# Optimization experiments

Measured on AMD Instinct MI355X. Metric: run time of the kernel, lower is better.

Reference implementation:

```python
import jax, jax.numpy as jnp
import numpy as np

N = 4096          # n_nodes
M = 8192          # m_nodes (= 2*N, required by block structure)
D = 128           # in_dim == hidden_dim (conv1 is reapplied to its own output)
H = 128
NUM_ITERS = 3


def setup_inputs() -> dict:
    key = jax.random.key(0)
    ks = jax.random.split(key, 6)
    X = jax.random.normal(ks[0], (N, D), dtype=jnp.float32)
    R = jax.random.uniform(ks[1], (N, N), dtype=jnp.float32)
    A = 0.5 * (R + R.T)  # symmetric, strictly positive connectivity matrix
    # upsample MLP: Linear(n_nodes -> m_nodes - n_nodes), torch weight layout [out, in]
    W_up = jax.random.normal(ks[2], (M - N, N), dtype=jnp.float32) * 0.02
    b_up = jnp.zeros((M - N,), dtype=jnp.float32)
    # GCNConv linear weights stored [in, out]
    W1 = jax.random.normal(ks[3], (D, H), dtype=jnp.float32) * 0.05
    b1 = jnp.zeros((H,), dtype=jnp.float32)
    W2 = jax.random.normal(ks[4], (H, H), dtype=jnp.float32) * 0.05
    b2 = jnp.zeros((H,), dtype=jnp.float32)
    return dict(X=X, A=A, W_up=W_up, b_up=b_up, W1=W1, b1=b1, W2=W2, b2=b2)


def _gcn(Adj, X, W, b):
    # PyG GCNConv on a fully dense, strictly-positive weighted graph:
    # every diagonal entry is nonzero, so add_remaining_self_loops is a no-op and
    # out = D^{-1/2} A D^{-1/2} (X W) + b  exactly.
    deg = Adj.sum(axis=0)                         # [m] column degree
    dinv = jnp.where(deg > 0, jax.lax.rsqrt(deg), 0.0)
    An = Adj * dinv[:, None] * dinv[None, :]      # symmetric normalization
    return An @ (X @ W) + b


def reference(X, A, W_up, b_up, W1, b1, W2, b2):
    # new_nodes = upsample_mlp(X.T).T  -> [M-N, D]
    new_nodes = (X.T @ W_up.T + b_up).T
    Xu = jnp.concatenate([X, new_nodes], axis=0)  # [M, D]
    # block adjacency: [[A, A.T], [A, sigmoid(new @ new.T)]]
    Adj = jnp.block([[A, A.T],
                     [A, jax.nn.sigmoid(new_nodes @ new_nodes.T)]])  # [M, M]
    A_out = Adj
    for _ in range(NUM_ITERS):
        Xu = jax.nn.relu(_gcn(Adj, Xu, W1, b1))
        Adj = jax.nn.sigmoid(Xu @ Xu.T)           # mid-loop adjacency rebuild
        Xu = jax.nn.relu(_gcn(Adj, Xu, W2, b2))
        A_out = jax.nn.sigmoid(Xu @ Xu.T)
        # NOTE: edge_index for the next conv1 is NOT rebuilt from A_out in the
        # original (only after conv1), so Adj carries the mid-loop matrix.
    return A_out
```

## Files before the change

### kernel.cpp

```cpp
#include <hip/hip_runtime.h>
#include <hip/hip_bf16.h>


#define N_NODES 4096
#define M_NODES 8192
#define DIM 128
#define SPLITS 8

typedef __attribute__((ext_vector_type(4))) float f32x4;
typedef __attribute__((ext_vector_type(8))) short bf16x8;

__device__ __forceinline__ unsigned short f2bf(float f) {
  union { float f; unsigned u; } v; v.f = f;
  unsigned r = v.u + 0x7fffu + ((v.u >> 16) & 1u);
  return (unsigned short)(r >> 16);
}

__device__ __forceinline__ void gld16(unsigned short* lds, const unsigned short* g) {
  __builtin_amdgcn_global_load_lds(
      (const __attribute__((address_space(1))) unsigned int*)g,
      (__attribute__((address_space(3))) unsigned int*)lds, 16, 0, 0);
}

__device__ __forceinline__ float sigmoidf_(float x) { return 1.0f / (1.0f + __expf(-x)); }


__global__ void cast_x_kernel(const float* __restrict__ X, unsigned short* __restrict__ Xu,
                              unsigned short* __restrict__ XT) {
  int idx = blockIdx.x * 256 + threadIdx.x;
  int i = idx >> 7, c = idx & 127;
  unsigned short b = f2bf(X[idx]);
  Xu[idx] = b;
  XT[(size_t)c * N_NODES + i] = b;
}

__global__ void cast_wup_kernel(const float4* __restrict__ W, ushort4* __restrict__ Wb) {
  int idx = blockIdx.x * 256 + threadIdx.x;
  float4 v = W[idx];
  ushort4 o;
  o.x = f2bf(v.x); o.y = f2bf(v.y); o.z = f2bf(v.z); o.w = f2bf(v.w);
  Wb[idx] = o;
}

__global__ void cast_wt_kernel(const float* __restrict__ W, unsigned short* __restrict__ WT) {
  int idx = blockIdx.x * 256 + threadIdx.x;
  int k = idx >> 7, c = idx & 127;
  WT[c * DIM + k] = f2bf(W[idx]);
}

__global__ void cast_a_kernel(const float* __restrict__ A, unsigned short* __restrict__ Adj,
                              float* __restrict__ colsumA) {
  int c = blockIdx.x * 256 + threadIdx.x;
  int r0 = blockIdx.y * 128;
  float s = 0.f;
  for (int r = 0; r < 128; ++r) {
    int row = r0 + r;
    float a = A[(size_t)row * N_NODES + c];
    unsigned short b = f2bf(a);
    Adj[(size_t)row * M_NODES + c] = b;
    Adj[(size_t)(row + N_NODES) * M_NODES + c] = b;
    Adj[(size_t)row * M_NODES + N_NODES + c] = b;
    s += a;
  }
  atomicAdd(&colsumA[c], s);
}

__global__ void init_deg_kernel(const float* __restrict__ colsumA, float* __restrict__ deg) {
  int i = blockIdx.x * 256 + threadIdx.x;
  deg[i] = (i < N_NODES) ? 2.0f * colsumA[i] : colsumA[i - N_NODES];
}

__global__ void dinv_kernel(const float* __restrict__ deg, float* __restrict__ dinv) {
  int i = blockIdx.x * 256 + threadIdx.x;
  float d = deg[i];
  dinv[i] = d > 0.f ? rsqrtf(d) : 0.f;
}


__global__ __launch_bounds__(256)
void gemm_split_kernel(const unsigned short* __restrict__ A, long lda,
                       const unsigned short* __restrict__ BT, long ldb,
                       float* __restrict__ accOut, int M, int kChunk) {
  __shared__ __align__(16) unsigned short lA[128 * 32];
  __shared__ __align__(16) unsigned short lB[128 * 32];
  const int t = threadIdx.x;
  const int w = t >> 6, lane = t & 63;
  const int q = lane >> 4, l15 = lane & 15;
  const int m0 = blockIdx.x * 128;
  const long k0b = (long)blockIdx.y * kChunk;
  const int arow = t >> 2, achk = t & 3;

  f32x4 acc[2][8];
#pragma unroll
  for (int a = 0; a < 2; ++a)
#pragma unroll
    for (int b = 0; b < 8; ++b) acc[a][b] = (f32x4)0.f;

  for (int ks = 0; ks < kChunk; ks += 32) {
    const long k0 = k0b + ks;
    __syncthreads();
    gld16(&lA[(size_t)t * 8], &A[(size_t)(m0 + arow) * lda + k0 + achk * 8]);
    gld16(&lA[2048 + (size_t)t * 8], &A[(size_t)(m0 + 64 + arow) * lda + k0 + achk * 8]);
    gld16(&lB[(size_t)t * 8], &BT[(size_t)arow * ldb + k0 + achk * 8]);
    gld16(&lB[2048 + (size_t)t * 8], &BT[(size_t)(64 + arow) * ldb + k0 + achk * 8]);
    __syncthreads();
    bf16x8 a0 = *(const bf16x8*)&lA[(w * 32 + l15) * 32 + q * 8];
    bf16x8 a1 = *(const bf16x8*)&lA[(w * 32 + 16 + l15) * 32 + q * 8];
#pragma unroll
    for (int nt = 0; nt < 8; ++nt) {
      bf16x8 b = *(const bf16x8*)&lB[(nt * 16 + l15) * 32 + q * 8];
      acc[0][nt] = __builtin_amdgcn_mfma_f32_16x16x32_bf16(a0, b, acc[0][nt], 0, 0, 0);
      acc[1][nt] = __builtin_amdgcn_mfma_f32_16x16x32_bf16(a1, b, acc[1][nt], 0, 0, 0);
    }
  }
  float* slice = accOut + (size_t)blockIdx.y * M * DIM;
#pragma unroll
  for (int mt = 0; mt < 2; ++mt)
#pragma unroll
    for (int nt = 0; nt < 8; ++nt)
#pragma unroll
      for (int i = 0; i < 4; ++i) {
        int row = m0 + w * 32 + mt * 16 + q * 4 + i;
        slice[(size_t)row * DIM + nt * 16 + l15] = acc[mt][nt][i];
      }
}

__global__ void reduce_acc_kernel(const float* __restrict__ acc, int M,
                                  unsigned short* __restrict__ dst,
                                  const float* __restrict__ bias_row,
                                  const float* __restrict__ bias_col,
                                  const float* __restrict__ dinv, int mode) {
  int idx = blockIdx.x * 256 + threadIdx.x;
  float s = 0.f;
#pragma unroll
  for (int sp = 0; sp < SPLITS; ++sp) s += acc[(size_t)sp * M * DIM + idx];
  int row = idx >> 7, c = idx & 127;
  float v;
  if (mode == 0) v = s + bias_row[row];
  else { v = dinv[row] * s + bias_col[c]; v = fmaxf(v, 0.f); }
  dst[idx] = f2bf(v);
}


template <int MODE>
__global__ __launch_bounds__(256)
void rebuild_kernel(const unsigned short* __restrict__ XA,
                    const unsigned short* __restrict__ XB,
                    void* __restrict__ out, long ldo, float* __restrict__ deg) {
  __shared__ __align__(16) unsigned short smem[32768];
  __shared__ float lcol[128];
  unsigned short* lA = smem;
  unsigned short* lB = smem + 16384;
  const int t = threadIdx.x, w = t >> 6, lane = t & 63;
  const int q = lane >> 4, l15 = lane & 15;
  const int i0 = blockIdx.x * 128, j0 = blockIdx.y * 128;
  const int srow = t >> 2, schk = t & 3;
#pragma unroll
  for (int kk = 0; kk < 4; ++kk)
#pragma unroll
    for (int h = 0; h < 2; ++h) {
      gld16(&lA[kk * 4096 + h * 2048 + t * 8],
            &XA[(size_t)(i0 + h * 64 + srow) * DIM + kk * 32 + schk * 8]);
      gld16(&lB[kk * 4096 + h * 2048 + t * 8],
            &XB[(size_t)(j0 + h * 64 + srow) * DIM + kk * 32 + schk * 8]);
    }
  if (MODE == 0 && t < 128) lcol[t] = 0.f;
  __syncthreads();

  f32x4 acc[2][8];
#pragma unroll
  for (int a = 0; a < 2; ++a)
#pragma unroll
    for (int b = 0; b < 8; ++b) acc[a][b] = (f32x4)0.f;

#pragma unroll
  for (int kk = 0; kk < 4; ++kk) {
    bf16x8 a0 = *(const bf16x8*)&lA[kk * 4096 + (w * 32 + l15) * 32 + q * 8];
    bf16x8 a1 = *(const bf16x8*)&lA[kk * 4096 + (w * 32 + 16 + l15) * 32 + q * 8];
#pragma unroll
    for (int nt = 0; nt < 8; ++nt) {
      bf16x8 b = *(const bf16x8*)&lB[kk * 4096 + (nt * 16 + l15) * 32 + q * 8];
      acc[0][nt] = __builtin_amdgcn_mfma_f32_16x16x32_bf16(a0, b, acc[0][nt], 0, 0, 0);
      acc[1][nt] = __builtin_amdgcn_mfma_f32_16x16x32_bf16(a1, b, acc[1][nt], 0, 0, 0);
    }
  }
  __syncthreads();

  if (MODE == 0) {
    unsigned short* lC = smem;
#pragma unroll
    for (int mt = 0; mt < 2; ++mt)
#pragma unroll
      for (int nt = 0; nt < 8; ++nt) {
        float cs = 0.f;
#pragma unroll
        for (int i = 0; i < 4; ++i) {
          float sv = sigmoidf_(acc[mt][nt][i]);
          cs += sv;
          lC[(w * 32 + mt * 16 + q * 4 + i) * 136 + nt * 16 + l15] = f2bf(sv);
        }
        cs += __shfl_xor(cs, 16);
        cs += __shfl_xor(cs, 32);
        if (lane < 16) atomicAdd(&lcol[nt * 16 + lane], cs);
      }
    __syncthreads();
    unsigned short* og = (unsigned short*)out;
#pragma unroll
    for (int cc = 0; cc < 8; ++cc) {
      int ch = t + cc * 256;
      int row = ch >> 4, c16 = ch & 15;
      *(bf16x8*)&og[(size_t)(i0 + row) * ldo + j0 + c16 * 8] =
          *(const bf16x8*)&lC[row * 136 + c16 * 8];
    }
    if (t < 128) atomicAdd(&deg[j0 + t], lcol[t]);
  } else {
    float* og = (float*)out;
#pragma unroll
    for (int mt = 0; mt < 2; ++mt)
#pragma unroll
      for (int nt = 0; nt < 8; ++nt)
#pragma unroll
        for (int i = 0; i < 4; ++i)
          og[(size_t)(i0 + w * 32 + mt * 16 + q * 4 + i) * ldo + j0 + nt * 16 + l15] =
              sigmoidf_(acc[mt][nt][i]);
  }
}


__global__ __launch_bounds__(256)
void yz_kernel(const unsigned short* __restrict__ Xu, const unsigned short* __restrict__ WT,
               const float* __restrict__ dinv, unsigned short* __restrict__ ZT, int ldz) {
  __shared__ __align__(16) unsigned short smem[32768];
  unsigned short* lA = smem;
  unsigned short* lB = smem + 16384;
  const int t = threadIdx.x, w = t >> 6, lane = t & 63;
  const int q = lane >> 4, l15 = lane & 15;
  const int r0 = blockIdx.x * 128;
  const int srow = t >> 2, schk = t & 3;
#pragma unroll
  for (int kk = 0; kk < 4; ++kk)
#pragma unroll
    for (int h = 0; h < 2; ++h) {
      gld16(&lA[kk * 4096 + h * 2048 + t * 8],
            &Xu[(size_t)(r0 + h * 64 + srow) * DIM + kk * 32 + schk * 8]);
      gld16(&lB[kk * 4096 + h * 2048 + t * 8],
            &WT[(size_t)(h * 64 + srow) * DIM + kk * 32 + schk * 8]);
    }
  __syncthreads();

  f32x4 acc[2][8];
#pragma unroll
  for (int a = 0; a < 2; ++a)
#pragma unroll
    for (int b = 0; b < 8; ++b) acc[a][b] = (f32x4)0.f;

#pragma unroll
  for (int kk = 0; kk < 4; ++kk) {
    bf16x8 a0 = *(const bf16x8*)&lA[kk * 4096 + (w * 32 + l15) * 32 + q * 8];
    bf16x8 a1 = *(const bf16x8*)&lA[kk * 4096 + (w * 32 + 16 + l15) * 32 + q * 8];
#pragma unroll
    for (int nt = 0; nt < 8; ++nt) {
      bf16x8 b = *(const bf16x8*)&lB[kk * 4096 + (nt * 16 + l15) * 32 + q * 8];
      acc[0][nt] = __builtin_amdgcn_mfma_f32_16x16x32_bf16(a0, b, acc[0][nt], 0, 0, 0);
      acc[1][nt] = __builtin_amdgcn_mfma_f32_16x16x32_bf16(a1, b, acc[1][nt], 0, 0, 0);
    }
  }
  __syncthreads();
  unsigned short* lT = smem;
#pragma unroll
  for (int mt = 0; mt < 2; ++mt)
#pragma unroll
    for (int nt = 0; nt < 8; ++nt)
#pragma unroll
      for (int i = 0; i < 4; ++i) {
        int r = w * 32 + mt * 16 + q * 4 + i;
        lT[(nt * 16 + l15) * 136 + r] = f2bf(dinv[r0 + r] * acc[mt][nt][i]);
      }
  __syncthreads();
#pragma unroll
  for (int cc = 0; cc < 8; ++cc) {
    int ch = t + cc * 256;
    int c = ch >> 4, c16 = ch & 15;
    *(bf16x8*)&ZT[(size_t)c * ldz + r0 + c16 * 8] = *(const bf16x8*)&lT[c * 136 + c16 * 8];
  }
}


extern "C" void kernel_launch(void* const* d_in, const int* in_sizes, int n_in,
                              void* d_out, int out_size, void* d_ws, size_t ws_size,
                              hipStream_t stream) {
  (void)in_sizes; (void)n_in; (void)out_size;
  const float* X   = (const float*)d_in[0];
  const float* A   = (const float*)d_in[1];
  const float* Wup = (const float*)d_in[2];
  const float* bup = (const float*)d_in[3];
  const float* W1  = (const float*)d_in[4];
  const float* b1  = (const float*)d_in[5];
  const float* W2  = (const float*)d_in[6];
  const float* b2  = (const float*)d_in[7];

  const size_t ADJ_BYTES = (size_t)M_NODES * M_NODES * 2;
  char* ws = (char*)d_ws;
  size_t off = 0;
  auto alloc = [&](size_t bytes) {
    char* p = ws + off;
    off += (bytes + 255) & ~(size_t)255;
    return p;
  };
  float*          accb    = (float*)alloc((size_t)SPLITS * M_NODES * DIM * 4);
  unsigned short* Xu      = (unsigned short*)alloc((size_t)M_NODES * DIM * 2);
  unsigned short* ZT      = (unsigned short*)alloc((size_t)DIM * M_NODES * 2);
  unsigned short* XT      = (unsigned short*)alloc((size_t)DIM * N_NODES * 2);
  unsigned short* W1T     = (unsigned short*)alloc(DIM * DIM * 2);
  unsigned short* W2T     = (unsigned short*)alloc(DIM * DIM * 2);
  float*          colsumA = (float*)alloc(N_NODES * 4);
  float*          deg     = (float*)alloc(M_NODES * 4);
  float*          dinv    = (float*)alloc(M_NODES * 4);

  unsigned short* Adj;
  if (ws_size >= off + ADJ_BYTES) Adj = (unsigned short*)(ws + off);
  else                            Adj = (unsigned short*)d_out;
  unsigned short* Wupb = Adj;

  unsigned short* XuNew = Xu + (size_t)N_NODES * DIM;

  hipMemsetAsync(colsumA, 0, N_NODES * 4, stream);
  cast_x_kernel<<<N_NODES * DIM / 256, 256, 0, stream>>>(X, Xu, XT);
  cast_wup_kernel<<<(N_NODES * (size_t)N_NODES / 4) / 256, 256, 0, stream>>>(
      (const float4*)Wup, (ushort4*)Wupb);
  cast_wt_kernel<<<64, 256, 0, stream>>>(W1, W1T);
  cast_wt_kernel<<<64, 256, 0, stream>>>(W2, W2T);

  gemm_split_kernel<<<dim3(N_NODES / 128, SPLITS), 256, 0, stream>>>(
      Wupb, N_NODES, XT, N_NODES, accb, N_NODES, N_NODES / SPLITS);
  reduce_acc_kernel<<<N_NODES * DIM / 256, 256, 0, stream>>>(
      accb, N_NODES, XuNew, bup, nullptr, nullptr, 0);

  cast_a_kernel<<<dim3(N_NODES / 256, N_NODES / 128), 256, 0, stream>>>(A, Adj, colsumA);
  init_deg_kernel<<<M_NODES / 256, 256, 0, stream>>>(colsumA, deg);
  rebuild_kernel<0><<<dim3(N_NODES / 128, N_NODES / 128), 256, 0, stream>>>(
      XuNew, XuNew, Adj + (size_t)N_NODES * M_NODES + N_NODES, M_NODES, deg + N_NODES);
  dinv_kernel<<<M_NODES / 256, 256, 0, stream>>>(deg, dinv);

  for (int it = 0; it < 3; ++it) {
    yz_kernel<<<M_NODES / 128, 256, 0, stream>>>(Xu, W1T, dinv, ZT, M_NODES);
    gemm_split_kernel<<<dim3(M_NODES / 128, SPLITS), 256, 0, stream>>>(
        Adj, M_NODES, ZT, M_NODES, accb, M_NODES, M_NODES / SPLITS);
    reduce_acc_kernel<<<M_NODES * DIM / 256, 256, 0, stream>>>(
        accb, M_NODES, Xu, nullptr, b1, dinv, 1);
    hipMemsetAsync(deg, 0, M_NODES * 4, stream);
    rebuild_kernel<0><<<dim3(M_NODES / 128, M_NODES / 128), 256, 0, stream>>>(
        Xu, Xu, Adj, M_NODES, deg);
    dinv_kernel<<<M_NODES / 256, 256, 0, stream>>>(deg, dinv);
    yz_kernel<<<M_NODES / 128, 256, 0, stream>>>(Xu, W2T, dinv, ZT, M_NODES);
    gemm_split_kernel<<<dim3(M_NODES / 128, SPLITS), 256, 0, stream>>>(
        Adj, M_NODES, ZT, M_NODES, accb, M_NODES, M_NODES / SPLITS);
    reduce_acc_kernel<<<M_NODES * DIM / 256, 256, 0, stream>>>(
        accb, M_NODES, Xu, nullptr, b2, dinv, 1);
    if (it == 2)
      rebuild_kernel<1><<<dim3(M_NODES / 128, M_NODES / 128), 256, 0, stream>>>(
          Xu, Xu, d_out, M_NODES, nullptr);
  }
}
```

Measured before the change: 1.006 ms.

## Exploit block structure of initial adjacency and register-stream aggregation GEMM

```diff
diff --git a/kernel.cpp b/kernel.cpp
--- a/kernel.cpp
+++ b/kernel.cpp
@@ -5,7 +5,7 @@
 #define N_NODES 4096
 #define M_NODES 8192
 #define DIM 128
-#define SPLITS 8
+#define SLICE_ELEMS ((size_t)M_NODES * DIM)
 
 typedef __attribute__((ext_vector_type(4))) float f32x4;
 typedef __attribute__((ext_vector_type(8))) short bf16x8;
@@ -15,6 +15,10 @@
   unsigned r = v.u + 0x7fffu + ((v.u >> 16) & 1u);
   return (unsigned short)(r >> 16);
 }
+__device__ __forceinline__ float bf2f(unsigned short b) {
+  union { unsigned u; float f; } v; v.u = ((unsigned)b) << 16;
+  return v.f;
+}
 
 __device__ __forceinline__ void gld16(unsigned short* lds, const unsigned short* g) {
   __builtin_amdgcn_global_load_lds(
@@ -48,18 +52,14 @@
   WT[c * DIM + k] = f2bf(W[idx]);
 }
 
-__global__ void cast_a_kernel(const float* __restrict__ A, unsigned short* __restrict__ Adj,
+__global__ void cast_a_kernel(const float* __restrict__ A, unsigned short* __restrict__ Ab,
                               float* __restrict__ colsumA) {
   int c = blockIdx.x * 256 + threadIdx.x;
   int r0 = blockIdx.y * 128;
   float s = 0.f;
   for (int r = 0; r < 128; ++r) {
-    int row = r0 + r;
-    float a = A[(size_t)row * N_NODES + c];
-    unsigned short b = f2bf(a);
-    Adj[(size_t)row * M_NODES + c] = b;
-    Adj[(size_t)(row + N_NODES) * M_NODES + c] = b;
-    Adj[(size_t)row * M_NODES + N_NODES + c] = b;
+    float a = A[(size_t)(r0 + r) * N_NODES + c];
+    Ab[(size_t)(r0 + r) * N_NODES + c] = f2bf(a);
     s += a;
   }
   atomicAdd(&colsumA[c], s);
@@ -76,19 +76,23 @@
   dinv[i] = d > 0.f ? rsqrtf(d) : 0.f;
 }
 
+__global__ void zsum_kernel(const unsigned short* __restrict__ ZT,
+                            unsigned short* __restrict__ ZsumT) {
+  int idx = blockIdx.x * 256 + threadIdx.x;
+  int c = idx >> 12, j = idx & 4095;
+  float v = bf2f(ZT[(size_t)c * M_NODES + j]) + bf2f(ZT[(size_t)c * M_NODES + N_NODES + j]);
+  ZsumT[idx] = f2bf(v);
+}
+
 
 __global__ __launch_bounds__(256)
-void gemm_split_kernel(const unsigned short* __restrict__ A, long lda,
-                       const unsigned short* __restrict__ BT, long ldb,
-                       float* __restrict__ accOut, int M, int kChunk) {
-  __shared__ __align__(16) unsigned short lA[128 * 32];
-  __shared__ __align__(16) unsigned short lB[128 * 32];
-  const int t = threadIdx.x;
-  const int w = t >> 6, lane = t & 63;
+void agg_kernel(const unsigned short* __restrict__ A, long lda,
+                const unsigned short* __restrict__ BT, long ldb,
+                float* __restrict__ accBase, int sliceOff, long rowOff, int kIters) {
+  const int t = threadIdx.x, w = t >> 6, lane = t & 63;
   const int q = lane >> 4, l15 = lane & 15;
-  const int m0 = blockIdx.x * 128;
-  const long k0b = (long)blockIdx.y * kChunk;
-  const int arow = t >> 2, achk = t & 3;
+  const long m0 = (long)blockIdx.x * 128;
+  const long kbase = (long)blockIdx.y * 32L * kIters;
 
   f32x4 acc[2][8];
 #pragma unroll
@@ -96,45 +100,56 @@
 #pragma unroll
     for (int b = 0; b < 8; ++b) acc[a][b] = (f32x4)0.f;
 
-  for (int ks = 0; ks < kChunk; ks += 32) {
-    const long k0 = k0b + ks;
-    __syncthreads();
-    gld16(&lA[(size_t)t * 8], &A[(size_t)(m0 + arow) * lda + k0 + achk * 8]);
-    gld16(&lA[2048 + (size_t)t * 8], &A[(size_t)(m0 + 64 + arow) * lda + k0 + achk * 8]);
-    gld16(&lB[(size_t)t * 8], &BT[(size_t)arow * ldb + k0 + achk * 8]);
-    gld16(&lB[2048 + (size_t)t * 8], &BT[(size_t)(64 + arow) * ldb + k0 + achk * 8]);
-    __syncthreads();
-    bf16x8 a0 = *(const bf16x8*)&lA[(w * 32 + l15) * 32 + q * 8];
-    bf16x8 a1 = *(const bf16x8*)&lA[(w * 32 + 16 + l15) * 32 + q * 8];
+  const size_t ar0 = (size_t)(m0 + w * 32 + l15) * lda + kbase + q * 8;
+  const size_t ar1 = ar0 + (size_t)16 * lda;
+  const size_t bbase = kbase + q * 8;
+
+  bf16x8 a0[2], a1[2], bf[2][8];
+
+#define LOADG(KT, S)                                                              \
+  do {                                                                            \
+    const size_t kk_ = (size_t)(KT) * 32;                                         \
+    a0[S] = *(const bf16x8*)&A[ar0 + kk_];                                        \
+    a1[S] = *(const bf16x8*)&A[ar1 + kk_];                                        \
+    _Pragma("unroll")                                                             \
+    for (int nt = 0; nt < 8; ++nt)                                                \
+      bf[S][nt] = *(const bf16x8*)&BT[(size_t)(nt * 16 + l15) * ldb + bbase + kk_];\
+  } while (0)
+
+  LOADG(0, 0);
+#pragma unroll 2
+  for (int kt = 0; kt < kIters; ++kt) {
+    const int cur = kt & 1, nxt = cur ^ 1;
+    if (kt + 1 < kIters) LOADG(kt + 1, nxt);
 #pragma unroll
     for (int nt = 0; nt < 8; ++nt) {
-      bf16x8 b = *(const bf16x8*)&lB[(nt * 16 + l15) * 32 + q * 8];
-      acc[0][nt] = __builtin_amdgcn_mfma_f32_16x16x32_bf16(a0, b, acc[0][nt], 0, 0, 0);
-      acc[1][nt] = __builtin_amdgcn_mfma_f32_16x16x32_bf16(a1, b, acc[1][nt], 0, 0, 0);
-    }
-  }
-  float* slice = accOut + (size_t)blockIdx.y * M * DIM;
+      acc[0][nt] = __builtin_amdgcn_mfma_f32_16x16x32_bf16(a0[cur], bf[cur][nt], acc[0][nt], 0, 0, 0);
+      acc[1][nt] = __builtin_amdgcn_mfma_f32_16x16x32_bf16(a1[cur], bf[cur][nt], acc[1][nt], 0, 0, 0);
+    }
+  }
+#undef LOADG
+
+  float* C = accBase + (size_t)(sliceOff + blockIdx.y) * SLICE_ELEMS + (size_t)(rowOff + m0) * DIM;
 #pragma unroll
   for (int mt = 0; mt < 2; ++mt)
 #pragma unroll
     for (int nt = 0; nt < 8; ++nt)
 #pragma unroll
-      for (int i = 0; i < 4; ++i) {
-        int row = m0 + w * 32 + mt * 16 + q * 4 + i;
-        slice[(size_t)row * DIM + nt * 16 + l15] = acc[mt][nt][i];
-      }
-}
-
-__global__ void reduce_acc_kernel(const float* __restrict__ acc, int M,
+      for (int i = 0; i < 4; ++i)
+        C[(size_t)(w * 32 + mt * 16 + q * 4 + i) * DIM + nt * 16 + l15] = acc[mt][nt][i];
+}
+
+__global__ void reduce_acc_kernel(const float* __restrict__ acc,
                                   unsigned short* __restrict__ dst,
                                   const float* __restrict__ bias_row,
                                   const float* __restrict__ bias_col,
-                                  const float* __restrict__ dinv, int mode) {
-  int idx = blockIdx.x * 256 + threadIdx.x;
+                                  const float* __restrict__ dinv, int mode,
+                                  int nLo, int nHi, int rowSplit) {
+  int idx = blockIdx.x * 256 + threadIdx.x;
+  int row = idx >> 7, c = idx & 127;
+  int ns = (row < rowSplit) ? nLo : nHi;
   float s = 0.f;
-#pragma unroll
-  for (int sp = 0; sp < SPLITS; ++sp) s += acc[(size_t)sp * M * DIM + idx];
-  int row = idx >> 7, c = idx & 127;
+  for (int sp = 0; sp < ns; ++sp) s += acc[(size_t)sp * SLICE_ELEMS + idx];
   float v;
   if (mode == 0) v = s + bias_row[row];
   else { v = dinv[row] * s + bias_col[c]; v = fmaxf(v, 0.f); }
@@ -307,15 +322,18 @@
     off += (bytes + 255) & ~(size_t)255;
     return p;
   };
-  float*          accb    = (float*)alloc((size_t)SPLITS * M_NODES * DIM * 4);
+  float*          accb    = (float*)alloc(16 * SLICE_ELEMS * 4);
   unsigned short* Xu      = (unsigned short*)alloc((size_t)M_NODES * DIM * 2);
   unsigned short* ZT      = (unsigned short*)alloc((size_t)DIM * M_NODES * 2);
   unsigned short* XT      = (unsigned short*)alloc((size_t)DIM * N_NODES * 2);
+  unsigned short* ZsumT   = (unsigned short*)alloc((size_t)DIM * N_NODES * 2);
   unsigned short* W1T     = (unsigned short*)alloc(DIM * DIM * 2);
   unsigned short* W2T     = (unsigned short*)alloc(DIM * DIM * 2);
   float*          colsumA = (float*)alloc(N_NODES * 4);
   float*          deg     = (float*)alloc(M_NODES * 4);
   float*          dinv    = (float*)alloc(M_NODES * 4);
+  unsigned short* Abf     = (unsigned short*)alloc((size_t)N_NODES * N_NODES * 2);
+  unsigned short* S0      = (unsigned short*)alloc((size_t)N_NODES * N_NODES * 2);
 
   unsigned short* Adj;
   if (ws_size >= off + ADJ_BYTES) Adj = (unsigned short*)(ws + off);
@@ -326,37 +344,50 @@
 
   hipMemsetAsync(colsumA, 0, N_NODES * 4, stream);
   cast_x_kernel<<<N_NODES * DIM / 256, 256, 0, stream>>>(X, Xu, XT);
-  cast_wup_kernel<<<(N_NODES * (size_t)N_NODES / 4) / 256, 256, 0, stream>>>(
+  cast_wup_kernel<<<((size_t)N_NODES * N_NODES / 4) / 256, 256, 0, stream>>>(
       (const float4*)Wup, (ushort4*)Wupb);
   cast_wt_kernel<<<64, 256, 0, stream>>>(W1, W1T);
   cast_wt_kernel<<<64, 256, 0, stream>>>(W2, W2T);
 
-  gemm_split_kernel<<<dim3(N_NODES / 128, SPLITS), 256, 0, stream>>>(
-      Wupb, N_NODES, XT, N_NODES, accb, N_NODES, N_NODES / SPLITS);
+  agg_kernel<<<dim3(N_NODES / 128, 8), 256, 0, stream>>>(
+      Wupb, N_NODES, XT, N_NODES, accb, 0, 0, 16);
   reduce_acc_kernel<<<N_NODES * DIM / 256, 256, 0, stream>>>(
-      accb, N_NODES, XuNew, bup, nullptr, nullptr, 0);
-
-  cast_a_kernel<<<dim3(N_NODES / 256, N_NODES / 128), 256, 0, stream>>>(A, Adj, colsumA);
+      accb, XuNew, bup, nullptr, nullptr, 0, 8, 8, N_NODES);
+
+  cast_a_kernel<<<dim3(N_NODES / 256, N_NODES / 128), 256, 0, stream>>>(A, Abf, colsumA);
   init_deg_kernel<<<M_NODES / 256, 256, 0, stream>>>(colsumA, deg);
   rebuild_kernel<0><<<dim3(N_NODES / 128, N_NODES / 128), 256, 0, stream>>>(
-      XuNew, XuNew, Adj + (size_t)N_NODES * M_NODES + N_NODES, M_NODES, deg + N_NODES);
+      XuNew, XuNew, S0, N_NODES, deg + N_NODES);
   dinv_kernel<<<M_NODES / 256, 256, 0, stream>>>(deg, dinv);
 
+  yz_kernel<<<M_NODES / 128, 256, 0, stream>>>(Xu, W1T, dinv, ZT, M_NODES);
+  zsum_kernel<<<DIM * N_NODES / 256, 256, 0, stream>>>(ZT, ZsumT);
+  agg_kernel<<<dim3(N_NODES / 128, 8), 256, 0, stream>>>(
+      Abf, N_NODES, ZsumT, N_NODES, accb, 0, 0, 16);
+  agg_kernel<<<dim3(N_NODES / 128, 8), 256, 0, stream>>>(
+      Abf, N_NODES, ZT, M_NODES, accb, 0, N_NODES, 16);
+  agg_kernel<<<dim3(N_NODES / 128, 8), 256, 0, stream>>>(
+      S0, N_NODES, ZT + N_NODES, M_NODES, accb, 8, N_NODES, 16);
+  reduce_acc_kernel<<<M_NODES * DIM / 256, 256, 0, stream>>>(
+      accb, Xu, nullptr, b1, dinv, 1, 8, 16, N_NODES);
+
   for (int it = 0; it < 3; ++it) {
-    yz_kernel<<<M_NODES / 128, 256, 0, stream>>>(Xu, W1T, dinv, ZT, M_NODES);
-    gemm_split_kernel<<<dim3(M_NODES / 128, SPLITS), 256, 0, stream>>>(
-        Adj, M_NODES, ZT, M_NODES, accb, M_NODES, M_NODES / SPLITS);
-    reduce_acc_kernel<<<M_NODES * DIM / 256, 256, 0, stream>>>(
-        accb, M_NODES, Xu, nullptr, b1, dinv, 1);
+    if (it > 0) {
+      yz_kernel<<<M_NODES / 128, 256, 0, stream>>>(Xu, W1T, dinv, ZT, M_NODES);
+      agg_kernel<<<dim3(M_NODES / 128, 8), 256, 0, stream>>>(
+          Adj, M_NODES, ZT, M_NODES, accb, 0, 0, 32);
+      reduce_acc_kernel<<<M_NODES * DIM / 256, 256, 0, stream>>>(
+          accb, Xu, nullptr, b1, dinv, 1, 8, 8, 0);
+    }
     hipMemsetAsync(deg, 0, M_NODES * 4, stream);
     rebuild_kernel<0><<<dim3(M_NODES / 128, M_NODES / 128), 256, 0, stream>>>(
         Xu, Xu, Adj, M_NODES, deg);
     dinv_kernel<<<M_NODES / 256, 256, 0, stream>>>(deg, dinv);
     yz_kernel<<<M_NODES / 128, 256, 0, stream>>>(Xu, W2T, dinv, ZT, M_NODES);
-    gemm_split_kernel<<<dim3(M_NODES / 128, SPLITS), 256, 0, stream>>>(
-        Adj, M_NODES, ZT, M_NODES, accb, M_NODES, M_NODES / SPLITS);
+    agg_kernel<<<dim3(M_NODES / 128, 8), 256, 0, stream>>>(
+        Adj, M_NODES, ZT, M_NODES, accb, 0, 0, 32);
     reduce_acc_kernel<<<M_NODES * DIM / 256, 256, 0, stream>>>(
-        accb, M_NODES, Xu, nullptr, b2, dinv, 1);
+        accb, Xu, nullptr, b2, dinv, 1, 8, 8, 0);
     if (it == 2)
       rebuild_kernel<1><<<dim3(M_NODES / 128, M_NODES / 128), 256, 0, stream>>>(
           Xu, Xu, d_out, M_NODES, nullptr);
```

After: 2.054 ms. +104.2%, slower.

## Store adjacency in pre-tiled MFMA-friendly layout and coalesce GEMM/rebuild outputs

Applied to the files above, without the earlier changes.

```diff
diff --git a/kernel.cpp b/kernel.cpp
--- a/kernel.cpp
+++ b/kernel.cpp
@@ -5,7 +5,7 @@
 #define N_NODES 4096
 #define M_NODES 8192
 #define DIM 128
-#define SPLITS 8
+#define SLICE_ELEMS ((size_t)M_NODES * DIM)
 
 typedef __attribute__((ext_vector_type(4))) float f32x4;
 typedef __attribute__((ext_vector_type(8))) short bf16x8;
@@ -34,12 +34,15 @@
   XT[(size_t)c * N_NODES + i] = b;
 }
 
-__global__ void cast_wup_kernel(const float4* __restrict__ W, ushort4* __restrict__ Wb) {
-  int idx = blockIdx.x * 256 + threadIdx.x;
-  float4 v = W[idx];
+__global__ void cast_wup_kernel(const float4* __restrict__ W, unsigned short* __restrict__ Wb) {
+  int idx4 = blockIdx.x * 256 + threadIdx.x;
+  int r = idx4 >> 10, c = (idx4 & 1023) << 2;
+  float4 v = W[idx4];
   ushort4 o;
   o.x = f2bf(v.x); o.y = f2bf(v.y); o.z = f2bf(v.z); o.w = f2bf(v.w);
-  Wb[idx] = o;
+  int tm = r >> 7, rr = r & 127;
+  int kc = c >> 10, st = (c & 1023) >> 5, e = c & 31;
+  *(ushort4*)&Wb[((size_t)tm * 4 + kc) * 131072 + (size_t)st * 4096 + rr * 32 + e] = o;
 }
 
 __global__ void cast_wt_kernel(const float* __restrict__ W, unsigned short* __restrict__ WT) {
@@ -52,14 +55,16 @@
                               float* __restrict__ colsumA) {
   int c = blockIdx.x * 256 + threadIdx.x;
   int r0 = blockIdx.y * 128;
+  int tm = r0 >> 7;
+  int kc = c >> 10, st = (c & 1023) >> 5, e = c & 31;
+  size_t a1 = ((size_t)(tm)      * 8 + kc)     * 131072 + (size_t)st * 4096 + e;
+  size_t a2 = ((size_t)(tm)      * 8 + 4 + kc) * 131072 + (size_t)st * 4096 + e;
+  size_t a3 = ((size_t)(tm + 32) * 8 + kc)     * 131072 + (size_t)st * 4096 + e;
   float s = 0.f;
   for (int r = 0; r < 128; ++r) {
-    int row = r0 + r;
-    float a = A[(size_t)row * N_NODES + c];
+    float a = A[(size_t)(r0 + r) * N_NODES + c];
     unsigned short b = f2bf(a);
-    Adj[(size_t)row * M_NODES + c] = b;
-    Adj[(size_t)(row + N_NODES) * M_NODES + c] = b;
-    Adj[(size_t)row * M_NODES + N_NODES + c] = b;
+    Adj[a1 + r * 32] = b; Adj[a2 + r * 32] = b; Adj[a3 + r * 32] = b;
     s += a;
   }
   atomicAdd(&colsumA[c], s);
@@ -77,17 +82,18 @@
 }
 
 
-__global__ __launch_bounds__(256)
-void gemm_split_kernel(const unsigned short* __restrict__ A, long lda,
-                       const unsigned short* __restrict__ BT, long ldb,
-                       float* __restrict__ accOut, int M, int kChunk) {
-  __shared__ __align__(16) unsigned short lA[128 * 32];
-  __shared__ __align__(16) unsigned short lB[128 * 32];
-  const int t = threadIdx.x;
-  const int w = t >> 6, lane = t & 63;
+__global__ __launch_bounds__(256, 2)
+void agg_kernel(const unsigned short* __restrict__ At, long tileRowElems,
+                const unsigned short* __restrict__ BT, long ldb,
+                float* __restrict__ accBase, int kIters) {
+  __shared__ __align__(16) unsigned short lA[4096];
+  __shared__ __align__(16) unsigned short lB[4096];
+  const int t = threadIdx.x, w = t >> 6, lane = t & 63;
   const int q = lane >> 4, l15 = lane & 15;
-  const int m0 = blockIdx.x * 128;
-  const long k0b = (long)blockIdx.y * kChunk;
+  const int sg0 = blockIdx.y * kIters;
+  const size_t abase = (size_t)blockIdx.x * tileRowElems +
+                       (size_t)(sg0 >> 5) * 131072 + (size_t)(sg0 & 31) * 4096;
+  const size_t bk = (size_t)sg0 * 32;
   const int arow = t >> 2, achk = t & 3;
 
   f32x4 acc[2][8];
@@ -96,13 +102,12 @@
 #pragma unroll
     for (int b = 0; b < 8; ++b) acc[a][b] = (f32x4)0.f;
 
-  for (int ks = 0; ks < kChunk; ks += 32) {
-    const long k0 = k0b + ks;
+  for (int s = 0; s < kIters; ++s) {
     __syncthreads();
-    gld16(&lA[(size_t)t * 8], &A[(size_t)(m0 + arow) * lda + k0 + achk * 8]);
-    gld16(&lA[2048 + (size_t)t * 8], &A[(size_t)(m0 + 64 + arow) * lda + k0 + achk * 8]);
-    gld16(&lB[(size_t)t * 8], &BT[(size_t)arow * ldb + k0 + achk * 8]);
-    gld16(&lB[2048 + (size_t)t * 8], &BT[(size_t)(64 + arow) * ldb + k0 + achk * 8]);
+    gld16(&lA[t * 8],        &At[abase + (size_t)s * 4096 + t * 8]);
+    gld16(&lA[2048 + t * 8], &At[abase + (size_t)s * 4096 + 2048 + t * 8]);
+    gld16(&lB[t * 8],        &BT[(size_t)arow * ldb + bk + s * 32 + achk * 8]);
+    gld16(&lB[2048 + t * 8], &BT[(size_t)(64 + arow) * ldb + bk + s * 32 + achk * 8]);
     __syncthreads();
     bf16x8 a0 = *(const bf16x8*)&lA[(w * 32 + l15) * 32 + q * 8];
     bf16x8 a1 = *(const bf16x8*)&lA[(w * 32 + 16 + l15) * 32 + q * 8];
@@ -113,32 +118,31 @@
       acc[1][nt] = __builtin_amdgcn_mfma_f32_16x16x32_bf16(a1, b, acc[1][nt], 0, 0, 0);
     }
   }
-  float* slice = accOut + (size_t)blockIdx.y * M * DIM;
+  float* ct = accBase + (size_t)blockIdx.y * SLICE_ELEMS + (size_t)blockIdx.x * 16384;
 #pragma unroll
   for (int mt = 0; mt < 2; ++mt)
 #pragma unroll
     for (int nt = 0; nt < 8; ++nt)
-#pragma unroll
-      for (int i = 0; i < 4; ++i) {
-        int row = m0 + w * 32 + mt * 16 + q * 4 + i;
-        slice[(size_t)row * DIM + nt * 16 + l15] = acc[mt][nt][i];
-      }
-}
-
-__global__ void reduce_acc_kernel(const float* __restrict__ acc, int M,
+      *(f32x4*)&ct[(((w * 2 + mt) * 8 + nt) * 256) + (q * 16 + l15) * 4] = acc[mt][nt];
+}
+
+__global__ void reduce_acc_kernel(const float* __restrict__ acc,
                                   unsigned short* __restrict__ dst,
                                   const float* __restrict__ bias_row,
                                   const float* __restrict__ bias_col,
-                                  const float* __restrict__ dinv, int mode) {
-  int idx = blockIdx.x * 256 + threadIdx.x;
+                                  const float* __restrict__ dinv, int mode, int nSlices) {
+  int p = blockIdx.x * 256 + threadIdx.x;
   float s = 0.f;
-#pragma unroll
-  for (int sp = 0; sp < SPLITS; ++sp) s += acc[(size_t)sp * M * DIM + idx];
-  int row = idx >> 7, c = idx & 127;
-  float v;
-  if (mode == 0) v = s + bias_row[row];
-  else { v = dinv[row] * s + bias_col[c]; v = fmaxf(v, 0.f); }
-  dst[idx] = f2bf(v);
+  for (int sp = 0; sp < nSlices; ++sp) s += acc[(size_t)sp * SLICE_ELEMS + p];
+  int tile = p >> 14, r = p & 16383;
+  int grp = r >> 8, r2 = r & 255;
+  int nt = grp & 7, wmt = grp >> 3;
+  int i = r2 & 3, ql = r2 >> 2;
+  int row = tile * 128 + (wmt >> 1) * 32 + (wmt & 1) * 16 + (ql >> 4) * 4 + i;
+  int col = nt * 16 + (ql & 15);
+  float v = (mode == 0) ? (s + bias_row[row])
+                        : fmaxf(dinv[row] * s + bias_col[col], 0.f);
+  dst[(size_t)row * DIM + col] = f2bf(v);
 }
 
 
@@ -146,7 +150,8 @@
 __global__ __launch_bounds__(256)
 void rebuild_kernel(const unsigned short* __restrict__ XA,
                     const unsigned short* __restrict__ XB,
-                    void* __restrict__ out, long ldo, float* __restrict__ deg) {
+                    void* __restrict__ out, long p1 ,
+                    long col0, float* __restrict__ deg) {
   __shared__ __align__(16) unsigned short smem[32768];
   __shared__ float lcol[128];
   unsigned short* lA = smem;
@@ -205,24 +210,42 @@
       }
     __syncthreads();
     unsigned short* og = (unsigned short*)out;
+    const long rowbase = p1 + i0, colbase = col0 + j0;
+    const size_t tb = ((size_t)(rowbase >> 7) * 8 + (colbase >> 10)) * 131072;
+    const int stb = (int)((colbase & 1023) >> 5);
 #pragma unroll
     for (int cc = 0; cc < 8; ++cc) {
       int ch = t + cc * 256;
       int row = ch >> 4, c16 = ch & 15;
-      *(bf16x8*)&og[(size_t)(i0 + row) * ldo + j0 + c16 * 8] =
+      *(bf16x8*)&og[tb + (size_t)(stb + (c16 >> 2)) * 4096 + row * 32 + (c16 & 3) * 8] =
           *(const bf16x8*)&lC[row * 136 + c16 * 8];
     }
-    if (t < 128) atomicAdd(&deg[j0 + t], lcol[t]);
+    if (t < 128) atomicAdd(&deg[colbase + t], lcol[t]);
   } else {
     float* og = (float*)out;
-#pragma unroll
-    for (int mt = 0; mt < 2; ++mt)
-#pragma unroll
-      for (int nt = 0; nt < 8; ++nt)
-#pragma unroll
-        for (int i = 0; i < 4; ++i)
-          og[(size_t)(i0 + w * 32 + mt * 16 + q * 4 + i) * ldo + j0 + nt * 16 + l15] =
-              sigmoidf_(acc[mt][nt][i]);
+    float* lCf = (float*)smem;
+#pragma unroll
+    for (int h2 = 0; h2 < 2; ++h2) {
+      __syncthreads();
+      if ((w >> 1) == h2) {
+#pragma unroll
+        for (int mt = 0; mt < 2; ++mt)
+#pragma unroll
+          for (int nt = 0; nt < 8; ++nt)
+#pragma unroll
+            for (int i = 0; i < 4; ++i)
+              lCf[((w & 1) * 32 + mt * 16 + q * 4 + i) * 128 + nt * 16 + l15] =
+                  sigmoidf_(acc[mt][nt][i]);
+      }
+      __syncthreads();
+#pragma unroll
+      for (int j = 0; j < 8; ++j) {
+        int ch = t + j * 256;
+        int r64 = ch >> 5, c4 = (ch & 31) * 4;
+        *(f32x4*)&og[(size_t)(i0 + h2 * 64 + r64) * p1 + j0 + c4] =
+            *(const f32x4*)&lCf[r64 * 128 + c4];
+      }
+    }
   }
 }
 
@@ -307,7 +330,7 @@
     off += (bytes + 255) & ~(size_t)255;
     return p;
   };
-  float*          accb    = (float*)alloc((size_t)SPLITS * M_NODES * DIM * 4);
+  float*          accb    = (float*)alloc(8 * SLICE_ELEMS * 4);
   unsigned short* Xu      = (unsigned short*)alloc((size_t)M_NODES * DIM * 2);
   unsigned short* ZT      = (unsigned short*)alloc((size_t)DIM * M_NODES * 2);
   unsigned short* XT      = (unsigned short*)alloc((size_t)DIM * N_NODES * 2);
@@ -326,39 +349,39 @@
 
   hipMemsetAsync(colsumA, 0, N_NODES * 4, stream);
   cast_x_kernel<<<N_NODES * DIM / 256, 256, 0, stream>>>(X, Xu, XT);
-  cast_wup_kernel<<<(N_NODES * (size_t)N_NODES / 4) / 256, 256, 0, stream>>>(
-      (const float4*)Wup, (ushort4*)Wupb);
+  cast_wup_kernel<<<((size_t)N_NODES * N_NODES / 4) / 256, 256, 0, stream>>>(
+      (const float4*)Wup, Wupb);
   cast_wt_kernel<<<64, 256, 0, stream>>>(W1, W1T);
   cast_wt_kernel<<<64, 256, 0, stream>>>(W2, W2T);
 
-  gemm_split_kernel<<<dim3(N_NODES / 128, SPLITS), 256, 0, stream>>>(
-      Wupb, N_NODES, XT, N_NODES, accb, N_NODES, N_NODES / SPLITS);
+  agg_kernel<<<dim3(N_NODES / 128, 8), 256, 0, stream>>>(
+      Wupb, 4L * 131072, XT, N_NODES, accb, 16);
   reduce_acc_kernel<<<N_NODES * DIM / 256, 256, 0, stream>>>(
-      accb, N_NODES, XuNew, bup, nullptr, nullptr, 0);
+      accb, XuNew, bup, nullptr, nullptr, 0, 8);
 
   cast_a_kernel<<<dim3(N_NODES / 256, N_NODES / 128), 256, 0, stream>>>(A, Adj, colsumA);
   init_deg_kernel<<<M_NODES / 256, 256, 0, stream>>>(colsumA, deg);
   rebuild_kernel<0><<<dim3(N_NODES / 128, N_NODES / 128), 256, 0, stream>>>(
-      XuNew, XuNew, Adj + (size_t)N_NODES * M_NODES + N_NODES, M_NODES, deg + N_NODES);
+      XuNew, XuNew, Adj, N_NODES, N_NODES, deg);
   dinv_kernel<<<M_NODES / 256, 256, 0, stream>>>(deg, dinv);
 
   for (int it = 0; it < 3; ++it) {
     yz_kernel<<<M_NODES / 128, 256, 0, stream>>>(Xu, W1T, dinv, ZT, M_NODES);
-    gemm_split_kernel<<<dim3(M_NODES / 128, SPLITS), 256, 0, stream>>>(
-        Adj, M_NODES, ZT, M_NODES, accb, M_NODES, M_NODES / SPLITS);
+    agg_kernel<<<dim3(M_NODES / 128, 8), 256, 0, stream>>>(
+        Adj, 8L * 131072, ZT, M_NODES, accb, 32);
     reduce_acc_kernel<<<M_NODES * DIM / 256, 256, 0, stream>>>(
-        accb, M_NODES, Xu, nullptr, b1, dinv, 1);
+        accb, Xu, nullptr, b1, dinv, 1, 8);
     hipMemsetAsync(deg, 0, M_NODES * 4, stream);
     rebuild_kernel<0><<<dim3(M_NODES / 128, M_NODES / 128), 256, 0, stream>>>(
-        Xu, Xu, Adj, M_NODES, deg);
+        Xu, Xu, Adj, 0, 0, deg);
     dinv_kernel<<<M_NODES / 256, 256, 0, stream>>>(deg, dinv);
     yz_kernel<<<M_NODES / 128, 256, 0, stream>>>(Xu, W2T, dinv, ZT, M_NODES);
-    gemm_split_kernel<<<dim3(M_NODES / 128, SPLITS), 256, 0, stream>>>(
-        Adj, M_NODES, ZT, M_NODES, accb, M_NODES, M_NODES / SPLITS);
+    agg_kernel<<<dim3(M_NODES / 128, 8), 256, 0, stream>>>(
+        Adj, 8L * 131072, ZT, M_NODES, accb, 32);
     reduce_acc_kernel<<<M_NODES * DIM / 256, 256, 0, stream>>>(
-        accb, M_NODES, Xu, nullptr, b2, dinv, 1);
+        accb, Xu, nullptr, b2, dinv, 1, 8);
     if (it == 2)
       rebuild_kernel<1><<<dim3(M_NODES / 128, M_NODES / 128), 256, 0, stream>>>(
-          Xu, Xu, d_out, M_NODES, nullptr);
-  }
-}
+          Xu, Xu, d_out, M_NODES, 0, nullptr);
+  }
+}
```

Result: no change. 989.2 us (-1.7%).
